# Optimization experiments

Hardware: AMD Instinct MI355X
Metric: run time of the kernel (lower is better)

## Reference

```python
import jax, jax.numpy as jnp
import numpy as np
import math

B, S, H, NH, NB = 2, 512, 128, 4, 2
D = H // NH
V_ITEMS, NCAT, NMETA, BAG, TSPAN = 50000, 1000, 16, 5, 256
EPS_EMB, EPS = 1e-5, 1e-8
NEG = -(2.0 ** 32) + 1.0


def _ln(x, g, b, eps):
    m = x.mean(-1, keepdims=True)
    v = ((x - m) ** 2).mean(-1, keepdims=True)
    return (x - m) / jnp.sqrt(v + eps) * g + b


def setup_inputs() -> dict:
    key = jax.random.key(0)
    ks = jax.random.split(key, 24)
    sc = 0.02
    inp = {}
    inp['input_ids'] = jax.random.randint(ks[0], (B, S), 0, V_ITEMS + 1)
    inp['metadata_seq'] = jax.random.normal(ks[1], (B, S, NMETA), jnp.float32)
    inp['category_seq'] = jax.random.randint(ks[2], (B, S, BAG), 0, NCAT + 1)
    inp['time_matrix'] = jax.random.randint(ks[3], (B, S, S), 0, TSPAN + 1)
    item = jax.random.normal(ks[4], (V_ITEMS + 1, H), jnp.float32) * sc
    inp['item_emb_w'] = item.at[0].set(0.0)  # padding_idx=0 cleared
    cat = jax.random.normal(ks[5], (NCAT + 1, H // 2), jnp.float32) * sc
    inp['cat_emb_w'] = cat.at[0].set(0.0)
    inp['num_W'] = jax.random.normal(ks[6], (H // 2, NMETA), jnp.float32) * sc
    inp['num_b'] = jnp.zeros((H // 2,), jnp.float32)
    inp['fusion_W'] = jax.random.normal(ks[7], (H, 2 * H), jnp.float32) * sc
    inp['fusion_b'] = jnp.zeros((H,), jnp.float32)
    inp['emb_ln_g'] = jnp.ones((H,), jnp.float32)
    inp['emb_ln_b'] = jnp.zeros((H,), jnp.float32)
    inp['pos_K_w'] = jax.random.normal(ks[8], (S, H), jnp.float32) * sc
    inp['pos_V_w'] = jax.random.normal(ks[9], (S, H), jnp.float32) * sc
    inp['time_K_w'] = jax.random.normal(ks[10], (TSPAN + 1, H), jnp.float32) * sc
    inp['time_V_w'] = jax.random.normal(ks[11], (TSPAN + 1, H), jnp.float32) * sc
    inp['attn_ln_g'] = jnp.ones((NB, H), jnp.float32)
    inp['attn_ln_b'] = jnp.zeros((NB, H), jnp.float32)
    inp['Q_W'] = jax.random.normal(ks[12], (NB, H, H), jnp.float32) * sc
    inp['Q_b'] = jnp.zeros((NB, H), jnp.float32)
    inp['K_W'] = jax.random.normal(ks[13], (NB, H, H), jnp.float32) * sc
    inp['K_b'] = jnp.zeros((NB, H), jnp.float32)
    inp['V_W'] = jax.random.normal(ks[14], (NB, H, H), jnp.float32) * sc
    inp['V_b'] = jnp.zeros((NB, H), jnp.float32)
    inp['fwd_ln_g'] = jnp.ones((NB, H), jnp.float32)
    inp['fwd_ln_b'] = jnp.zeros((NB, H), jnp.float32)
    inp['w1_W'] = jax.random.normal(ks[15], (NB, H, H), jnp.float32) * sc
    inp['w1_b'] = jnp.zeros((NB, H), jnp.float32)
    inp['w2_W'] = jax.random.normal(ks[16], (NB, H, H), jnp.float32) * sc
    inp['w2_b'] = jnp.zeros((NB, H), jnp.float32)
    inp['last_ln_g'] = jnp.ones((H,), jnp.float32)
    inp['last_ln_b'] = jnp.zeros((H,), jnp.float32)
    return inp


def reference(input_ids, metadata_seq, category_seq, time_matrix, item_emb_w,
              cat_emb_w, num_W, num_b, fusion_W, fusion_b, emb_ln_g, emb_ln_b,
              pos_K_w, pos_V_w, time_K_w, time_V_w, attn_ln_g, attn_ln_b,
              Q_W, Q_b, K_W, K_b, V_W, V_b, fwd_ln_g, fwd_ln_b,
              w1_W, w1_b, w2_W, w2_b, last_ln_g, last_ln_b):
    # ---- seq2vec ----
    item_v = item_emb_w[input_ids] * math.sqrt(H)            # [B,S,H]
    bag_mask = (category_seq != 0)                           # EmbeddingBag mean, padding_idx=0
    cat_e = cat_emb_w[category_seq] * bag_mask[..., None]    # [B,S,BAG,H/2]
    cat_v = cat_e.sum(-2) / jnp.maximum(bag_mask.sum(-1, keepdims=True), 1)
    num_v = metadata_seq @ num_W.T + num_b                   # [B,S,H/2]
    comb = jnp.concatenate([item_v, num_v, cat_v], axis=-1)  # [B,S,2H]
    vecs = _ln(comb @ fusion_W.T + fusion_b, emb_ln_g, emb_ln_b, EPS_EMB)

    # ---- vec2feats ----
    posK = pos_K_w.reshape(S, NH, D)
    posV = pos_V_w.reshape(S, NH, D)
    tK = time_K_w[time_matrix].reshape(B, S, S, NH, D)       # [B,S,S,h,d]
    tV = time_V_w[time_matrix].reshape(B, S, S, NH, D)
    timeline = (input_ids == 0)                              # [B,S]
    keep = (~timeline)[..., None].astype(vecs.dtype)
    vecs = vecs * keep
    causal = ~jnp.tril(jnp.ones((S, S), bool))               # mask where j > i
    inv_sqrt_d = 1.0 / math.sqrt(D)

    for i in range(NB):
        Qn = _ln(vecs, attn_ln_g[i], attn_ln_b[i], EPS)
        Q = (Qn @ Q_W[i].T + Q_b[i]).reshape(B, S, NH, D)
        K = (vecs @ K_W[i].T + K_b[i]).reshape(B, S, NH, D)
        V = (vecs @ V_W[i].T + V_b[i]).reshape(B, S, NH, D)
        aw = jnp.einsum('bihd,bjhd->bhij', Q, K)
        aw = aw + jnp.einsum('bihd,jhd->bhij', Q, posK)
        aw = aw + jnp.einsum('bijhd,bihd->bhij', tK, Q)
        aw = aw * inv_sqrt_d
        aw = jnp.where(timeline[:, None, :, None], NEG, aw)  # masks query rows (as in torch)
        aw = jnp.where(causal[None, None], NEG, aw)
        aw = jax.nn.softmax(aw, axis=-1)
        out = jnp.einsum('bhij,bjhd->bihd', aw, V)
        out = out + jnp.einsum('bhij,jhd->bihd', aw, posV)
        out = out + jnp.einsum('bhij,bijhd->bihd', aw, tV)
        out = out.reshape(B, S, H)
        vecs = Qn + out
        vecs = _ln(vecs, fwd_ln_g[i], fwd_ln_b[i], EPS)
        h1 = jax.nn.gelu(vecs @ w1_W[i].T + w1_b[i], approximate=False)
        vecs = vecs + (h1 @ w2_W[i].T + w2_b[i])
        vecs = vecs * keep

    return _ln(vecs, last_ln_g, last_ln_b, EPS)
```

## Files before the change

### kernel.cpp

```cpp
#include <hip/hip_runtime.h>
#include <hip/hip_cooperative_groups.h>
#include <math.h>

namespace cg = cooperative_groups;

#define Bn 2
#define Sn 512
#define Hn 128
#define NHn 4
#define Dn 32
#define BAGn 5
#define NMETAn 16
#define ROWS 1024
#define NBn 2
#define Tt 257

#define NEGF (-4294967295.0f)
#define INV_SQRT_D 0.17677669529663687f
#define SQRT_H 11.313708498984761f
#define EPS_EMB 1e-5f
#define EPSF 1e-8f

#define OFF_QN    0
#define OFF_Q     131072
#define OFF_K     262144
#define OFF_V     393216
#define OFF_O     524288

static __device__ __forceinline__ float red64(float v) {
#pragma unroll
    for (int m = 1; m < 64; m <<= 1) v += __shfl_xor(v, m, 64);
    return v;
}
static __device__ __forceinline__ float red64max(float v) {
#pragma unroll
    for (int m = 1; m < 64; m <<= 1) v = fmaxf(v, __shfl_xor(v, m, 64));
    return v;
}

static __device__ __forceinline__ void embed2(
    int r0, int t, float* sm,
    const int* __restrict__ ids, const float* __restrict__ meta,
    const int* __restrict__ cats,
    const float* __restrict__ item_w, const float* __restrict__ cat_w,
    const float* __restrict__ numW, const float* __restrict__ numb,
    const float* __restrict__ fusW, const float* __restrict__ fusb,
    const float* __restrict__ elng, const float* __restrict__ elnb,
    const float* __restrict__ alng, const float* __restrict__ alnb,
    const float* __restrict__ QW, const float* __restrict__ Qb,
    const float* __restrict__ KW, const float* __restrict__ Kb,
    const float* __restrict__ VW, const float* __restrict__ Vb,
    const float* __restrict__ posK, const float* __restrict__ posV,
    float* __restrict__ Qn, float* __restrict__ Q,
    float* __restrict__ K, float* __restrict__ V)
{
    float* combs = sm;
    float* xs    = sm + 512;
    float* qs    = sm + 768;
    float* parts = sm + 1024;
    float* pk    = sm + 1280;
    float* pv    = sm + 1536;
    float* wsum  = sm + 1792;
    int*   idl   = (int*)(sm + 1800);

    if (t < 2) idl[t] = ids[r0 + t];
    __syncthreads();
    { int r = t >> 7, c = t & 127; combs[r * 256 + c] = item_w[idl[r] * Hn + c] * SQRT_H; }
    if (t < 128) {
        int r = t >> 6, c = t & 63;
        float acc = numb[c];
#pragma unroll
        for (int m2 = 0; m2 < NMETAn; ++m2)
            acc += meta[(r0 + r) * NMETAn + m2] * numW[c * NMETAn + m2];
        combs[r * 256 + 128 + c] = acc;
    } else {
        int u = t - 128, r = u >> 6, c = u & 63;
        float ca = 0.f; int cnt = 0;
#pragma unroll
        for (int k2 = 0; k2 < BAGn; ++k2) {
            int cc2 = cats[(r0 + r) * BAGn + k2];
            if (cc2 != 0) { ca += cat_w[cc2 * 64 + c]; cnt++; }
        }
        combs[r * 256 + 192 + c] = ca / (float)(cnt > 0 ? cnt : 1);
    }
    __syncthreads();
    int h = t & 127, kh = t >> 7;
    {
        const float4* w4p = (const float4*)(fusW + h * 256 + kh * 128);
        const float* c0 = combs + kh * 128;
        const float* c1 = combs + 256 + kh * 128;
        float a0 = 0.f, a1 = 0.f, b0 = 0.f, b1 = 0.f;
#pragma unroll 16
        for (int k4 = 0; k4 < 32; ++k4) {
            float4 w4 = w4p[k4];
            int k = k4 * 4;
            a0 += c0[k] * w4.x + c0[k + 1] * w4.y;
            a1 += c0[k + 2] * w4.z + c0[k + 3] * w4.w;
            b0 += c1[k] * w4.x + c1[k + 1] * w4.y;
            b1 += c1[k + 2] * w4.z + c1[k + 3] * w4.w;
        }
        float A0 = a0 + a1, A1 = b0 + b1;
        if (kh) { parts[h] = A0; parts[128 + h] = A1; }
        __syncthreads();
        if (!kh) {
            xs[h] = A0 + parts[h] + fusb[h];
            xs[128 + h] = A1 + parts[128 + h] + fusb[h];
        }
    }
    __syncthreads();
    int w_ = t >> 6, row = w_ >> 1, l = t & 63, ch = ((w_ & 1) << 6) + l;
    float x = xs[row * 128 + ch];
    float s1 = red64(x);
    if (l == 0) wsum[w_] = s1;
    __syncthreads();
    float mean = (wsum[row * 2] + wsum[row * 2 + 1]) * (1.f / 128.f);
    float dlt = x - mean;
    float s2 = red64(dlt * dlt);
    if (l == 0) wsum[4 + w_] = s2;
    __syncthreads();
    float rstd = rsqrtf((wsum[4 + row * 2] + wsum[4 + row * 2 + 1]) * (1.f / 128.f) + EPS_EMB);
    float xv = dlt * rstd * elng[ch] + elnb[ch];
    xv = (idl[row] == 0) ? 0.f : xv;
    __syncthreads();
    xs[row * 128 + ch] = xv;
    __syncthreads();
    s1 = red64(xv);
    if (l == 0) wsum[w_] = s1;
    __syncthreads();
    mean = (wsum[row * 2] + wsum[row * 2 + 1]) * (1.f / 128.f);
    dlt = xv - mean;
    s2 = red64(dlt * dlt);
    if (l == 0) wsum[4 + w_] = s2;
    __syncthreads();
    rstd = rsqrtf((wsum[4 + row * 2] + wsum[4 + row * 2 + 1]) * (1.f / 128.f) + EPSF);
    float qn = dlt * rstd * alng[ch] + alnb[ch];
    qs[row * 128 + ch] = qn;
    Qn[(r0 + row) * 128 + ch] = qn;
    __syncthreads();
    {
        const float4* qw4 = (const float4*)(QW + h * 128 + kh * 64);
        const float4* kw4 = (const float4*)(KW + h * 128 + kh * 64);
        const float4* vw4 = (const float4*)(VW + h * 128 + kh * 64);
        const float* q0p = qs + kh * 64;
        const float* q1p = qs + 128 + kh * 64;
        const float* x0p = xs + kh * 64;
        const float* x1p = xs + 128 + kh * 64;
        float aq0 = 0, aq1 = 0, ak0 = 0, ak1 = 0, av0 = 0, av1 = 0;
#pragma unroll 8
        for (int k4 = 0; k4 < 16; ++k4) {
            float4 wq = qw4[k4], wk = kw4[k4], wv = vw4[k4];
            int k = k4 * 4;
            aq0 += q0p[k] * wq.x + q0p[k + 1] * wq.y + q0p[k + 2] * wq.z + q0p[k + 3] * wq.w;
            aq1 += q1p[k] * wq.x + q1p[k + 1] * wq.y + q1p[k + 2] * wq.z + q1p[k + 3] * wq.w;
            ak0 += x0p[k] * wk.x + x0p[k + 1] * wk.y + x0p[k + 2] * wk.z + x0p[k + 3] * wk.w;
            ak1 += x1p[k] * wk.x + x1p[k + 1] * wk.y + x1p[k + 2] * wk.z + x1p[k + 3] * wk.w;
            av0 += x0p[k] * wv.x + x0p[k + 1] * wv.y + x0p[k + 2] * wv.z + x0p[k + 3] * wv.w;
            av1 += x1p[k] * wv.x + x1p[k + 1] * wv.y + x1p[k + 2] * wv.z + x1p[k + 3] * wv.w;
        }
        if (kh) {
            parts[h] = aq0; parts[128 + h] = aq1;
            pk[h] = ak0; pk[128 + h] = ak1;
            pv[h] = av0; pv[128 + h] = av1;
        }
        __syncthreads();
        if (!kh) {
            int s0 = r0 & (Sn - 1), s1_ = (r0 + 1) & (Sn - 1);
            Q[r0 * 128 + h]       = aq0 + parts[h]       + Qb[h];
            Q[(r0 + 1) * 128 + h] = aq1 + parts[128 + h] + Qb[h];
            K[r0 * 128 + h]       = ak0 + pk[h]          + Kb[h] + posK[s0 * 128 + h];
            K[(r0 + 1) * 128 + h] = ak1 + pk[128 + h]    + Kb[h] + posK[s1_ * 128 + h];
            V[r0 * 128 + h]       = av0 + pv[h]          + Vb[h] + posV[s0 * 128 + h];
            V[(r0 + 1) * 128 + h] = av1 + pv[128 + h]    + Vb[h] + posV[s1_ * 128 + h];
        }
    }
}

static __device__ __forceinline__ void attn_phase(
    int b, int h, int i0, int t,
    const int* __restrict__ ids, const int* __restrict__ tmat,
    const float* __restrict__ Q, const float* __restrict__ K,
    const float* __restrict__ V,
    const float* __restrict__ tKw, const float* __restrict__ tVw,
    float* __restrict__ O,
    float* Kt, float* Vt, float* Stile, int* trowT,
    float* QTl, float* ql, int* tlf)
{
    __syncthreads();
    if (t < 4) tlf[t] = (ids[b * Sn + i0 + t] == 0) ? 1 : 0;
    if (t < 128) {
        int q_ = t >> 5, d = t & 31;
        ql[q_ * 33 + d] = Q[(b * Sn + i0 + q_) * Hn + h * 32 + d];
    }
    __syncthreads();

    for (int tt = t; tt < Tt; tt += 256) {
        const float4* tk4 = (const float4*)(tKw + tt * Hn + h * 32);
        float a0 = 0.f, a1 = 0.f, a2 = 0.f, a3 = 0.f;
#pragma unroll
        for (int dv = 0; dv < 8; ++dv) {
            float4 w4 = tk4[dv];
            int d = dv * 4;
            a0 += ql[d] * w4.x + ql[d + 1] * w4.y + ql[d + 2] * w4.z + ql[d + 3] * w4.w;
            a1 += ql[33 + d] * w4.x + ql[34 + d] * w4.y + ql[35 + d] * w4.z + ql[36 + d] * w4.w;
            a2 += ql[66 + d] * w4.x + ql[67 + d] * w4.y + ql[68 + d] * w4.z + ql[69 + d] * w4.w;
            a3 += ql[99 + d] * w4.x + ql[100 + d] * w4.y + ql[101 + d] * w4.z + ql[102 + d] * w4.w;
        }
        QTl[tt] = a0; QTl[260 + tt] = a1; QTl[520 + tt] = a2; QTl[780 + tt] = a3;
    }

    int tl_any = tlf[0] | tlf[1] | tlf[2] | tlf[3];
    int ntiles = tl_any ? 8 : ((i0 + 3) >> 6) + 1;

    int iq = t >> 6, jj = t & 63;
    int i_g = i0 + iq;
    int my_tl = tlf[iq];
    const int* trow = tmat + (b * Sn + i_g) * Sn;

    float qreg[32];
#pragma unroll
    for (int d = 0; d < 32; ++d) qreg[d] = ql[iq * 33 + d];

    int jq = jj >> 5, d = jj & 31;
    float m = -INFINITY, lsum = 0.f, acc = 0.f;

    for (int jt = 0; jt < ntiles; ++jt) {
        int j0 = jt * 64;
        __syncthreads();
        for (int f = t; f < 64 * 8; f += 256) {
            int jl = f >> 3, dv = f & 7;
            const float* src = K + (b * Sn + j0 + jl) * Hn + h * 32 + dv * 4;
            float4 w4 = *(const float4*)src;
            float* kd = &Kt[jl * 33 + dv * 4];
            kd[0] = w4.x; kd[1] = w4.y; kd[2] = w4.z; kd[3] = w4.w;
            float4 v4 = *(const float4*)(V + (b * Sn + j0 + jl) * Hn + h * 32 + dv * 4);
            float* vd = &Vt[jl * 33 + dv * 4];
            vd[0] = v4.x; vd[1] = v4.y; vd[2] = v4.z; vd[3] = v4.w;
        }
        __syncthreads();

        int active = my_tl || (j0 <= i_g);
        if (active) {
            int j = j0 + jj;
            float sv = NEGF;
            int tv = trow[j];
            if (!my_tl && j <= i_g) {
                float a = 0.f;
#pragma unroll
                for (int dd = 0; dd < 32; ++dd)
                    a += qreg[dd] * Kt[jj * 33 + dd];
                sv = (a + QTl[iq * 260 + tv]) * INV_SQRT_D;
            }
            float mt = red64max(sv);
            float mnew = fmaxf(m, mt);
            float alpha = expf(m - mnew);
            float p = expf(sv - mnew);
            lsum = lsum * alpha + red64(p);
            m = mnew;
            acc *= alpha;
            Stile[iq * 64 + jj] = p;
            trowT[iq * 64 + jj] = tv;
        }
        __syncthreads();
        if (active) {
            int base = jq * 32;
#pragma unroll 8
            for (int jl = base; jl < base + 32; ++jl) {
                float pp = Stile[iq * 64 + jl];
                int tv2 = trowT[iq * 64 + jl];
                acc += pp * (Vt[jl * 33 + d] + tVw[tv2 * Hn + h * 32 + d]);
            }
        }
    }

    float a2 = acc + __shfl_xor(acc, 32, 64);
    if (jj < 32)
        O[(b * Sn + i_g) * Hn + h * 32 + d] = a2 / lsum;
}

static __device__ __forceinline__ void ffn2(
    int r0, int t, float* sm,
    const int* __restrict__ ids, float* __restrict__ Qn,
    const float* __restrict__ O,
    const float* __restrict__ flng, const float* __restrict__ flnb,
    const float* __restrict__ w1W, const float* __restrict__ w1b,
    const float* __restrict__ w2W, const float* __restrict__ w2b,
    const float* __restrict__ alng, const float* __restrict__ alnb,
    const float* __restrict__ QW, const float* __restrict__ Qb,
    const float* __restrict__ KW, const float* __restrict__ Kb,
    const float* __restrict__ VW, const float* __restrict__ Vb,
    const float* __restrict__ posK, const float* __restrict__ posV,
    float* __restrict__ Q, float* __restrict__ K, float* __restrict__ V,
    const float* __restrict__ llng, const float* __restrict__ llnb,
    float* __restrict__ out, int nb, int last)
{
    float* ys    = sm;
    float* h1s   = sm + 256;
    float* parts = sm + 512;
    float* pk    = sm + 768;
    float* pv    = sm + 1024;
    float* wsum  = sm + 1280;

    ys[t] = Qn[r0 * 128 + t] + O[r0 * 128 + t];
    __syncthreads();
    int w_ = t >> 6, row = w_ >> 1, l = t & 63, ch = ((w_ & 1) << 6) + l;
    float x = ys[row * 128 + ch];
    float s1 = red64(x);
    if (l == 0) wsum[w_] = s1;
    __syncthreads();
    float mean = (wsum[row * 2] + wsum[row * 2 + 1]) * (1.f / 128.f);
    float dlt = x - mean;
    float s2 = red64(dlt * dlt);
    if (l == 0) wsum[4 + w_] = s2;
    __syncthreads();
    float rstd = rsqrtf((wsum[4 + row * 2] + wsum[4 + row * 2 + 1]) * (1.f / 128.f) + EPSF);
    float yv = dlt * rstd * flng[nb * 128 + ch] + flnb[nb * 128 + ch];
    __syncthreads();
    ys[row * 128 + ch] = yv;
    __syncthreads();

    int h = t & 127, kh = t >> 7;
    {
        const float4* w4p = (const float4*)(w1W + nb * 16384 + h * 128 + kh * 64);
        const float* y0 = ys + kh * 64;
        const float* y1 = ys + 128 + kh * 64;
        float a0 = 0.f, a1 = 0.f, b0 = 0.f, b1 = 0.f;
#pragma unroll 16
        for (int k4 = 0; k4 < 16; ++k4) {
            float4 w4 = w4p[k4];
            int k = k4 * 4;
            a0 += y0[k] * w4.x + y0[k + 1] * w4.y;
            a1 += y0[k + 2] * w4.z + y0[k + 3] * w4.w;
            b0 += y1[k] * w4.x + y1[k + 1] * w4.y;
            b1 += y1[k + 2] * w4.z + y1[k + 3] * w4.w;
        }
        float A0 = a0 + a1, A1 = b0 + b1;
        if (kh) { parts[h] = A0; parts[128 + h] = A1; }
        __syncthreads();
        if (!kh) {
            float v0 = A0 + parts[h] + w1b[nb * 128 + h];
            float v1 = A1 + parts[128 + h] + w1b[nb * 128 + h];
            h1s[h] = 0.5f * v0 * (1.f + erff(v0 * 0.70710678118654752f));
            h1s[128 + h] = 0.5f * v1 * (1.f + erff(v1 * 0.70710678118654752f));
        }
    }
    __syncthreads();
    {
        const float4* w4p = (const float4*)(w2W + nb * 16384 + h * 128 + kh * 64);
        const float* y0 = h1s + kh * 64;
        const float* y1 = h1s + 128 + kh * 64;
        float a0 = 0.f, a1 = 0.f, b0 = 0.f, b1 = 0.f;
#pragma unroll 16
        for (int k4 = 0; k4 < 16; ++k4) {
            float4 w4 = w4p[k4];
            int k = k4 * 4;
            a0 += y0[k] * w4.x + y0[k + 1] * w4.y;
            a1 += y0[k + 2] * w4.z + y0[k + 3] * w4.w;
            b0 += y1[k] * w4.x + y1[k + 1] * w4.y;
            b1 += y1[k + 2] * w4.z + y1[k + 3] * w4.w;
        }
        float A0 = a0 + a1, A1 = b0 + b1;
        __syncthreads();
        if (kh) { parts[h] = A0; parts[128 + h] = A1; }
        __syncthreads();
        if (!kh) {
            float z0 = A0 + parts[h] + w2b[nb * 128 + h] + ys[h];
            float z1 = A1 + parts[128 + h] + w2b[nb * 128 + h] + ys[128 + h];
            z0 = (ids[r0] == 0) ? 0.f : z0;
            z1 = (ids[r0 + 1] == 0) ? 0.f : z1;
            h1s[h] = z0; h1s[128 + h] = z1;
        }
    }
    __syncthreads();

    if (last) {
        x = h1s[row * 128 + ch];
        s1 = red64(x);
        if (l == 0) wsum[w_] = s1;
        __syncthreads();
        mean = (wsum[row * 2] + wsum[row * 2 + 1]) * (1.f / 128.f);
        dlt = x - mean;
        s2 = red64(dlt * dlt);
        if (l == 0) wsum[4 + w_] = s2;
        __syncthreads();
        rstd = rsqrtf((wsum[4 + row * 2] + wsum[4 + row * 2 + 1]) * (1.f / 128.f) + EPSF);
        out[(r0 + row) * 128 + ch] = dlt * rstd * llng[ch] + llnb[ch];
        return;
    }

    int nq = nb + 1;
    x = h1s[row * 128 + ch];
    s1 = red64(x);
    if (l == 0) wsum[w_] = s1;
    __syncthreads();
    mean = (wsum[row * 2] + wsum[row * 2 + 1]) * (1.f / 128.f);
    dlt = x - mean;
    s2 = red64(dlt * dlt);
    if (l == 0) wsum[4 + w_] = s2;
    __syncthreads();
    rstd = rsqrtf((wsum[4 + row * 2] + wsum[4 + row * 2 + 1]) * (1.f / 128.f) + EPSF);
    float qn = dlt * rstd * alng[nq * 128 + ch] + alnb[nq * 128 + ch];
    __syncthreads();
    ys[row * 128 + ch] = qn;
    Qn[(r0 + row) * 128 + ch] = qn;
    __syncthreads();

    {
        const float4* qw4 = (const float4*)(QW + nq * 16384 + h * 128 + kh * 64);
        const float4* kw4 = (const float4*)(KW + nq * 16384 + h * 128 + kh * 64);
        const float4* vw4 = (const float4*)(VW + nq * 16384 + h * 128 + kh * 64);
        const float* q0p = ys + kh * 64;
        const float* q1p = ys + 128 + kh * 64;
        const float* x0p = h1s + kh * 64;
        const float* x1p = h1s + 128 + kh * 64;
        float aq0 = 0, aq1 = 0, ak0 = 0, ak1 = 0, av0 = 0, av1 = 0;
#pragma unroll 8
        for (int k4 = 0; k4 < 16; ++k4) {
            float4 wq = qw4[k4], wk = kw4[k4], wv = vw4[k4];
            int k = k4 * 4;
            aq0 += q0p[k] * wq.x + q0p[k + 1] * wq.y + q0p[k + 2] * wq.z + q0p[k + 3] * wq.w;
            aq1 += q1p[k] * wq.x + q1p[k + 1] * wq.y + q1p[k + 2] * wq.z + q1p[k + 3] * wq.w;
            ak0 += x0p[k] * wk.x + x0p[k + 1] * wk.y + x0p[k + 2] * wk.z + x0p[k + 3] * wk.w;
            ak1 += x1p[k] * wk.x + x1p[k + 1] * wk.y + x1p[k + 2] * wk.z + x1p[k + 3] * wk.w;
            av0 += x0p[k] * wv.x + x0p[k + 1] * wv.y + x0p[k + 2] * wv.z + x0p[k + 3] * wv.w;
            av1 += x1p[k] * wv.x + x1p[k + 1] * wv.y + x1p[k + 2] * wv.z + x1p[k + 3] * wv.w;
        }
        if (kh) {
            parts[h] = aq0; parts[128 + h] = aq1;
            pk[h] = ak0; pk[128 + h] = ak1;
            pv[h] = av0; pv[128 + h] = av1;
        }
        __syncthreads();
        if (!kh) {
            int s0 = r0 & (Sn - 1), s1_ = (r0 + 1) & (Sn - 1);
            Q[r0 * 128 + h]       = aq0 + parts[h]       + Qb[nq * 128 + h];
            Q[(r0 + 1) * 128 + h] = aq1 + parts[128 + h] + Qb[nq * 128 + h];
            K[r0 * 128 + h]       = ak0 + pk[h]          + Kb[nq * 128 + h] + posK[s0 * 128 + h];
            K[(r0 + 1) * 128 + h] = ak1 + pk[128 + h]    + Kb[nq * 128 + h] + posK[s1_ * 128 + h];
            V[r0 * 128 + h]       = av0 + pv[h]          + Vb[nq * 128 + h] + posV[s0 * 128 + h];
            V[(r0 + 1) * 128 + h] = av1 + pv[128 + h]    + Vb[nq * 128 + h] + posV[s1_ * 128 + h];
        }
    }
}

__global__ __launch_bounds__(256, 2) void fused_kernel(
    const int* __restrict__ ids, const float* __restrict__ meta,
    const int* __restrict__ cats, const int* __restrict__ tmat,
    const float* __restrict__ item_w, const float* __restrict__ cat_w,
    const float* __restrict__ numW, const float* __restrict__ numb,
    const float* __restrict__ fusW, const float* __restrict__ fusb,
    const float* __restrict__ elng, const float* __restrict__ elnb,
    const float* __restrict__ posK, const float* __restrict__ posV,
    const float* __restrict__ tKw, const float* __restrict__ tVw,
    const float* __restrict__ alng, const float* __restrict__ alnb,
    const float* __restrict__ QW, const float* __restrict__ Qb,
    const float* __restrict__ KW, const float* __restrict__ Kb,
    const float* __restrict__ VW, const float* __restrict__ Vb,
    const float* __restrict__ flng, const float* __restrict__ flnb,
    const float* __restrict__ w1W, const float* __restrict__ w1b,
    const float* __restrict__ w2W, const float* __restrict__ w2b,
    const float* __restrict__ llng, const float* __restrict__ llnb,
    float* __restrict__ Qn, float* __restrict__ Q, float* __restrict__ K,
    float* __restrict__ V, float* __restrict__ O, float* __restrict__ out)
{
    cg::grid_group grid = cg::this_grid();
    __shared__ __align__(16) float sm[5912];
    int blk = blockIdx.x, t = threadIdx.x;
    int b8 = blk >> 6, j = blk & 63;
    int ab = b8 >> 2, ah = b8 & 3;

    embed2(blk * 2, t, sm, ids, meta, cats, item_w, cat_w, numW, numb,
           fusW, fusb, elng, elnb, alng, alnb, QW, Qb, KW, Kb, VW, Vb,
           posK, posV, Qn, Q, K, V);
    grid.sync();

    for (int nb = 0; nb < NBn; ++nb) {
        attn_phase(ab, ah, j * 4, t, ids, tmat, Q, K, V, tKw, tVw, O,
                   sm, sm + 2112, sm + 4224, (int*)(sm + 4480),
                   sm + 4736, sm + 5776, (int*)(sm + 5908));
        attn_phase(ab, ah, (127 - j) * 4, t, ids, tmat, Q, K, V, tKw, tVw, O,
                   sm, sm + 2112, sm + 4224, (int*)(sm + 4480),
                   sm + 4736, sm + 5776, (int*)(sm + 5908));
        grid.sync();
        ffn2(blk * 2, t, sm, ids, Qn, O, flng, flnb, w1W, w1b, w2W, w2b,
             alng, alnb, QW, Qb, KW, Kb, VW, Vb, posK, posV,
             Q, K, V, llng, llnb, out, nb, (nb == NBn - 1) ? 1 : 0);
        if (nb == 0) grid.sync();
    }
}

__global__ __launch_bounds__(256) void embed_qkv_kernel(
    const int* ids, const float* meta, const int* cats,
    const float* item_w, const float* cat_w, const float* numW, const float* numb,
    const float* fusW, const float* fusb, const float* elng, const float* elnb,
    const float* alng, const float* alnb,
    const float* QW, const float* Qb, const float* KW, const float* Kb,
    const float* VW, const float* Vb, const float* posK, const float* posV,
    float* Qn, float* Q, float* K, float* V)
{
    __shared__ __align__(16) float sm[1802];
    embed2(blockIdx.x * 2, threadIdx.x, sm, ids, meta, cats, item_w, cat_w,
           numW, numb, fusW, fusb, elng, elnb, alng, alnb, QW, Qb, KW, Kb,
           VW, Vb, posK, posV, Qn, Q, K, V);
}

__global__ __launch_bounds__(256) void attn_kernel(
    const int* ids, const int* tmat,
    const float* Q, const float* K, const float* V,
    const float* tKw, const float* tVw, float* O)
{
    __shared__ __align__(16) float sm[5912];
    int blk = blockIdx.x, t = threadIdx.x;
    int bh = blk & 7;
    int s  = blk >> 3;
    int g = s >> 5, r = s & 31;
    int mm;
    if      (g == 0) mm = r;
    else if (g == 1) mm = 127 - r;
    else if (g == 2) mm = 32 + r;
    else             mm = 95 - r;
    int b = bh >> 2, h = bh & 3;
    attn_phase(b, h, mm * 4, t, ids, tmat, Q, K, V, tKw, tVw, O,
               sm, sm + 2112, sm + 4224, (int*)(sm + 4480),
               sm + 4736, sm + 5776, (int*)(sm + 5908));
}

__global__ __launch_bounds__(256) void ffn_qkv_kernel(
    const int* ids, float* Qn, const float* O,
    const float* flng, const float* flnb,
    const float* w1W, const float* w1b, const float* w2W, const float* w2b,
    const float* alng, const float* alnb,
    const float* QW, const float* Qb, const float* KW, const float* Kb,
    const float* VW, const float* Vb, const float* posK, const float* posV,
    float* Q, float* K, float* V,
    const float* llng, const float* llnb, float* out, int nb, int last)
{
    __shared__ __align__(16) float sm[1288];
    ffn2(blockIdx.x * 2, threadIdx.x, sm, ids, Qn, O, flng, flnb, w1W, w1b,
         w2W, w2b, alng, alnb, QW, Qb, KW, Kb, VW, Vb, posK, posV,
         Q, K, V, llng, llnb, out, nb, last);
}

static int g_mode = -1;

extern "C" void kernel_launch(void* const* d_in, const int* in_sizes, int n_in,
                              void* d_out, int out_size, void* d_ws, size_t ws_size,
                              hipStream_t stream) {
    const int*   ids   = (const int*)  d_in[0];
    const float* meta  = (const float*)d_in[1];
    const int*   cats  = (const int*)  d_in[2];
    const int*   tmat  = (const int*)  d_in[3];
    const float* itemw = (const float*)d_in[4];
    const float* catw  = (const float*)d_in[5];
    const float* numW  = (const float*)d_in[6];
    const float* numb  = (const float*)d_in[7];
    const float* fusW  = (const float*)d_in[8];
    const float* fusb  = (const float*)d_in[9];
    const float* elng  = (const float*)d_in[10];
    const float* elnb  = (const float*)d_in[11];
    const float* posK  = (const float*)d_in[12];
    const float* posV  = (const float*)d_in[13];
    const float* tKw   = (const float*)d_in[14];
    const float* tVw   = (const float*)d_in[15];
    const float* alng  = (const float*)d_in[16];
    const float* alnb  = (const float*)d_in[17];
    const float* QW    = (const float*)d_in[18];
    const float* Qb    = (const float*)d_in[19];
    const float* KW    = (const float*)d_in[20];
    const float* Kb    = (const float*)d_in[21];
    const float* VW    = (const float*)d_in[22];
    const float* Vb    = (const float*)d_in[23];
    const float* flng  = (const float*)d_in[24];
    const float* flnb  = (const float*)d_in[25];
    const float* w1W   = (const float*)d_in[26];
    const float* w1b   = (const float*)d_in[27];
    const float* w2W   = (const float*)d_in[28];
    const float* w2b   = (const float*)d_in[29];
    const float* llng  = (const float*)d_in[30];
    const float* llnb  = (const float*)d_in[31];
    (void)in_sizes; (void)n_in; (void)out_size; (void)ws_size;

    float* ws = (float*)d_ws;
    float* Qnp = ws + OFF_QN;
    float* Qp  = ws + OFF_Q;
    float* Kp  = ws + OFF_K;
    float* Vp  = ws + OFF_V;
    float* Op  = ws + OFF_O;
    float* outp = (float*)d_out;

    if (g_mode < 0) {
        int dev = 0;
        (void)hipGetDevice(&dev);
        int coop = 0;
        (void)hipDeviceGetAttribute(&coop, hipDeviceAttributeCooperativeLaunch, dev);
        int ncu = 0;
        (void)hipDeviceGetAttribute(&ncu, hipDeviceAttributeMultiprocessorCount, dev);
        int maxb = 0;
        hipError_t oe = hipOccupancyMaxActiveBlocksPerMultiprocessor(
            &maxb, fused_kernel, 256, 0);
        g_mode = (coop && oe == hipSuccess && (long)maxb * (long)ncu >= 512) ? 1 : 0;
    }

    if (g_mode == 1) {
        void* args[] = {
            (void*)&ids, (void*)&meta, (void*)&cats, (void*)&tmat,
            (void*)&itemw, (void*)&catw, (void*)&numW, (void*)&numb,
            (void*)&fusW, (void*)&fusb, (void*)&elng, (void*)&elnb,
            (void*)&posK, (void*)&posV, (void*)&tKw, (void*)&tVw,
            (void*)&alng, (void*)&alnb, (void*)&QW, (void*)&Qb,
            (void*)&KW, (void*)&Kb, (void*)&VW, (void*)&Vb,
            (void*)&flng, (void*)&flnb, (void*)&w1W, (void*)&w1b,
            (void*)&w2W, (void*)&w2b, (void*)&llng, (void*)&llnb,
            (void*)&Qnp, (void*)&Qp, (void*)&Kp, (void*)&Vp, (void*)&Op,
            (void*)&outp
        };
        hipError_t e = hipLaunchCooperativeKernel((void*)fused_kernel,
                                                  dim3(512), dim3(256),
                                                  args, 0, stream);
        if (e == hipSuccess) return;
        g_mode = 0;
    }

    embed_qkv_kernel<<<ROWS / 2, 256, 0, stream>>>(
        ids, meta, cats, itemw, catw, numW, numb, fusW, fusb, elng, elnb,
        alng, alnb, QW, Qb, KW, Kb, VW, Vb, posK, posV, Qnp, Qp, Kp, Vp);
    for (int nb = 0; nb < NBn; ++nb) {
        attn_kernel<<<1024, 256, 0, stream>>>(ids, tmat, Qp, Kp, Vp, tKw, tVw, Op);
        ffn_qkv_kernel<<<ROWS / 2, 256, 0, stream>>>(
            ids, Qnp, Op, flng, flnb, w1W, w1b, w2W, w2b,
            alng, alnb, QW, Qb, KW, Kb, VW, Vb, posK, posV,
            Qp, Kp, Vp, llng, llnb, outp, nb, (nb == NBn - 1) ? 1 : 0);
    }
}
```

Baseline: 258.5 us.

## Use one row per block and 1024-block cooperative grid with shuffle-based attention

```diff
diff --git a/kernel.cpp b/kernel.cpp
--- a/kernel.cpp
+++ b/kernel.cpp
@@ -38,8 +38,71 @@
     return v;
 }
 
-static __device__ __forceinline__ void embed2(
-    int r0, int t, float* sm,
+static __device__ __forceinline__ float ln128(float x, int t, float* wsum, float eps) {
+    int w_ = t >> 6;
+    float s1 = red64(x);
+    if ((t & 63) == 0) wsum[w_] = s1;
+    __syncthreads();
+    float mean = (wsum[0] + wsum[1]) * (1.f / 128.f);
+    float dlt = x - mean;
+    float s2 = red64(dlt * dlt);
+    if ((t & 63) == 0) wsum[4 + w_] = s2;
+    __syncthreads();
+    float rstd = rsqrtf((wsum[4] + wsum[5]) * (1.f / 128.f) + eps);
+    return dlt * rstd;
+}
+
+static __device__ __forceinline__ float gemv_half(const float* __restrict__ W,
+                                                  const float* src, int h, int kh) {
+    const float4* w4p = (const float4*)(W + h * 128 + kh * 64);
+    const float* y0 = src + kh * 64;
+    float a0 = 0.f, a1 = 0.f;
+#pragma unroll 16
+    for (int k4 = 0; k4 < 16; ++k4) {
+        float4 w4 = w4p[k4];
+        int k = k4 * 4;
+        a0 += y0[k] * w4.x + y0[k + 1] * w4.y;
+        a1 += y0[k + 2] * w4.z + y0[k + 3] * w4.w;
+    }
+    return a0 + a1;
+}
+
+static __device__ __forceinline__ void qkv_row(
+    int row, int t, const float* qs, const float* xsrc,
+    float* parts, float* pk, float* pv,
+    const float* __restrict__ QW, const float* __restrict__ Qb,
+    const float* __restrict__ KW, const float* __restrict__ Kb,
+    const float* __restrict__ VW, const float* __restrict__ Vb,
+    const float* __restrict__ posK, const float* __restrict__ posV,
+    float* __restrict__ Q, float* __restrict__ K, float* __restrict__ V, int nq)
+{
+    int h = t & 127, kh = t >> 7;
+    const float4* qw4 = (const float4*)(QW + nq * 16384 + h * 128 + kh * 64);
+    const float4* kw4 = (const float4*)(KW + nq * 16384 + h * 128 + kh * 64);
+    const float4* vw4 = (const float4*)(VW + nq * 16384 + h * 128 + kh * 64);
+    const float* q0p = qs + kh * 64;
+    const float* x0p = xsrc + kh * 64;
+    float aq0 = 0.f, ak0 = 0.f, av0 = 0.f;
+#pragma unroll 8
+    for (int k4 = 0; k4 < 16; ++k4) {
+        float4 wq = qw4[k4], wk = kw4[k4], wv = vw4[k4];
+        int k = k4 * 4;
+        aq0 += q0p[k] * wq.x + q0p[k + 1] * wq.y + q0p[k + 2] * wq.z + q0p[k + 3] * wq.w;
+        ak0 += x0p[k] * wk.x + x0p[k + 1] * wk.y + x0p[k + 2] * wk.z + x0p[k + 3] * wk.w;
+        av0 += x0p[k] * wv.x + x0p[k + 1] * wv.y + x0p[k + 2] * wv.z + x0p[k + 3] * wv.w;
+    }
+    if (kh) { parts[h] = aq0; pk[h] = ak0; pv[h] = av0; }
+    __syncthreads();
+    if (!kh) {
+        int s0 = row & (Sn - 1);
+        Q[row * Hn + h] = aq0 + parts[h] + Qb[nq * Hn + h];
+        K[row * Hn + h] = ak0 + pk[h] + Kb[nq * Hn + h] + posK[s0 * Hn + h];
+        V[row * Hn + h] = av0 + pv[h] + Vb[nq * Hn + h] + posV[s0 * Hn + h];
+    }
+}
+
+static __device__ __forceinline__ void embed_row(
+    int row, int t, float* sm,
     const int* __restrict__ ids, const float* __restrict__ meta,
     const int* __restrict__ cats,
     const float* __restrict__ item_w, const float* __restrict__ cat_w,
@@ -55,230 +118,72 @@
     float* __restrict__ K, float* __restrict__ V)
 {
     float* combs = sm;
-    float* xs    = sm + 512;
-    float* qs    = sm + 768;
-    float* parts = sm + 1024;
-    float* pk    = sm + 1280;
-    float* pv    = sm + 1536;
-    float* wsum  = sm + 1792;
-    int*   idl   = (int*)(sm + 1800);
-
-    if (t < 2) idl[t] = ids[r0 + t];
-    __syncthreads();
-    { int r = t >> 7, c = t & 127; combs[r * 256 + c] = item_w[idl[r] * Hn + c] * SQRT_H; }
+    float* xs    = sm + 256;
+    float* qs    = sm + 384;
+    float* parts = sm + 512;
+    float* pk    = sm + 640;
+    float* pv    = sm + 768;
+    float* wsum  = sm + 896;
+
+    int id = ids[row];
+    int ch = t & 127, kh = t >> 7, h = ch;
+
     if (t < 128) {
-        int r = t >> 6, c = t & 63;
+        combs[t] = item_w[id * Hn + t] * SQRT_H;
+    } else if (t < 192) {
+        int c = t - 128;
         float acc = numb[c];
 #pragma unroll
         for (int m2 = 0; m2 < NMETAn; ++m2)
-            acc += meta[(r0 + r) * NMETAn + m2] * numW[c * NMETAn + m2];
-        combs[r * 256 + 128 + c] = acc;
+            acc += meta[row * NMETAn + m2] * numW[c * NMETAn + m2];
+        combs[128 + c] = acc;
     } else {
-        int u = t - 128, r = u >> 6, c = u & 63;
+        int c = t - 192;
         float ca = 0.f; int cnt = 0;
 #pragma unroll
         for (int k2 = 0; k2 < BAGn; ++k2) {
-            int cc2 = cats[(r0 + r) * BAGn + k2];
+            int cc2 = cats[row * BAGn + k2];
             if (cc2 != 0) { ca += cat_w[cc2 * 64 + c]; cnt++; }
         }
-        combs[r * 256 + 192 + c] = ca / (float)(cnt > 0 ? cnt : 1);
-    }
-    __syncthreads();
-    int h = t & 127, kh = t >> 7;
+        combs[192 + c] = ca / (float)(cnt > 0 ? cnt : 1);
+    }
+    __syncthreads();
+
+    float A0;
     {
         const float4* w4p = (const float4*)(fusW + h * 256 + kh * 128);
         const float* c0 = combs + kh * 128;
-        const float* c1 = combs + 256 + kh * 128;
-        float a0 = 0.f, a1 = 0.f, b0 = 0.f, b1 = 0.f;
+        float a0 = 0.f, a1 = 0.f;
 #pragma unroll 16
         for (int k4 = 0; k4 < 32; ++k4) {
             float4 w4 = w4p[k4];
             int k = k4 * 4;
             a0 += c0[k] * w4.x + c0[k + 1] * w4.y;
             a1 += c0[k + 2] * w4.z + c0[k + 3] * w4.w;
-            b0 += c1[k] * w4.x + c1[k + 1] * w4.y;
-            b1 += c1[k + 2] * w4.z + c1[k + 3] * w4.w;
         }
-        float A0 = a0 + a1, A1 = b0 + b1;
-        if (kh) { parts[h] = A0; parts[128 + h] = A1; }
-        __syncthreads();
-        if (!kh) {
-            xs[h] = A0 + parts[h] + fusb[h];
-            xs[128 + h] = A1 + parts[128 + h] + fusb[h];
-        }
-    }
-    __syncthreads();
-    int w_ = t >> 6, row = w_ >> 1, l = t & 63, ch = ((w_ & 1) << 6) + l;
-    float x = xs[row * 128 + ch];
-    float s1 = red64(x);
-    if (l == 0) wsum[w_] = s1;
-    __syncthreads();
-    float mean = (wsum[row * 2] + wsum[row * 2 + 1]) * (1.f / 128.f);
-    float dlt = x - mean;
-    float s2 = red64(dlt * dlt);
-    if (l == 0) wsum[4 + w_] = s2;
-    __syncthreads();
-    float rstd = rsqrtf((wsum[4 + row * 2] + wsum[4 + row * 2 + 1]) * (1.f / 128.f) + EPS_EMB);
-    float xv = dlt * rstd * elng[ch] + elnb[ch];
-    xv = (idl[row] == 0) ? 0.f : xv;
-    __syncthreads();
-    xs[row * 128 + ch] = xv;
-    __syncthreads();
-    s1 = red64(xv);
-    if (l == 0) wsum[w_] = s1;
-    __syncthreads();
-    mean = (wsum[row * 2] + wsum[row * 2 + 1]) * (1.f / 128.f);
-    dlt = xv - mean;
-    s2 = red64(dlt * dlt);
-    if (l == 0) wsum[4 + w_] = s2;
-    __syncthreads();
-    rstd = rsqrtf((wsum[4 + row * 2] + wsum[4 + row * 2 + 1]) * (1.f / 128.f) + EPSF);
-    float qn = dlt * rstd * alng[ch] + alnb[ch];
-    qs[row * 128 + ch] = qn;
-    Qn[(r0 + row) * 128 + ch] = qn;
-    __syncthreads();
-    {
-        const float4* qw4 = (const float4*)(QW + h * 128 + kh * 64);
-        const float4* kw4 = (const float4*)(KW + h * 128 + kh * 64);
-        const float4* vw4 = (const float4*)(VW + h * 128 + kh * 64);
-        const float* q0p = qs + kh * 64;
-        const float* q1p = qs + 128 + kh * 64;
-        const float* x0p = xs + kh * 64;
-        const float* x1p = xs + 128 + kh * 64;
-        float aq0 = 0, aq1 = 0, ak0 = 0, ak1 = 0, av0 = 0, av1 = 0;
-#pragma unroll 8
-        for (int k4 = 0; k4 < 16; ++k4) {
-            float4 wq = qw4[k4], wk = kw4[k4], wv = vw4[k4];
-            int k = k4 * 4;
-            aq0 += q0p[k] * wq.x + q0p[k + 1] * wq.y + q0p[k + 2] * wq.z + q0p[k + 3] * wq.w;
-            aq1 += q1p[k] * wq.x + q1p[k + 1] * wq.y + q1p[k + 2] * wq.z + q1p[k + 3] * wq.w;
-            ak0 += x0p[k] * wk.x + x0p[k + 1] * wk.y + x0p[k + 2] * wk.z + x0p[k + 3] * wk.w;
-            ak1 += x1p[k] * wk.x + x1p[k + 1] * wk.y + x1p[k + 2] * wk.z + x1p[k + 3] * wk.w;
-            av0 += x0p[k] * wv.x + x0p[k + 1] * wv.y + x0p[k + 2] * wv.z + x0p[k + 3] * wv.w;
-            av1 += x1p[k] * wv.x + x1p[k + 1] * wv.y + x1p[k + 2] * wv.z + x1p[k + 3] * wv.w;
-        }
-        if (kh) {
-            parts[h] = aq0; parts[128 + h] = aq1;
-            pk[h] = ak0; pk[128 + h] = ak1;
-            pv[h] = av0; pv[128 + h] = av1;
-        }
-        __syncthreads();
-        if (!kh) {
-            int s0 = r0 & (Sn - 1), s1_ = (r0 + 1) & (Sn - 1);
-            Q[r0 * 128 + h]       = aq0 + parts[h]       + Qb[h];
-            Q[(r0 + 1) * 128 + h] = aq1 + parts[128 + h] + Qb[h];
-            K[r0 * 128 + h]       = ak0 + pk[h]          + Kb[h] + posK[s0 * 128 + h];
-            K[(r0 + 1) * 128 + h] = ak1 + pk[128 + h]    + Kb[h] + posK[s1_ * 128 + h];
-            V[r0 * 128 + h]       = av0 + pv[h]          + Vb[h] + posV[s0 * 128 + h];
-            V[(r0 + 1) * 128 + h] = av1 + pv[128 + h]    + Vb[h] + posV[s1_ * 128 + h];
-        }
-    }
-}
-
-static __device__ __forceinline__ void attn_phase(
-    int b, int h, int i0, int t,
-    const int* __restrict__ ids, const int* __restrict__ tmat,
-    const float* __restrict__ Q, const float* __restrict__ K,
-    const float* __restrict__ V,
-    const float* __restrict__ tKw, const float* __restrict__ tVw,
-    float* __restrict__ O,
-    float* Kt, float* Vt, float* Stile, int* trowT,
-    float* QTl, float* ql, int* tlf)
-{
-    __syncthreads();
-    if (t < 4) tlf[t] = (ids[b * Sn + i0 + t] == 0) ? 1 : 0;
-    if (t < 128) {
-        int q_ = t >> 5, d = t & 31;
-        ql[q_ * 33 + d] = Q[(b * Sn + i0 + q_) * Hn + h * 32 + d];
-    }
-    __syncthreads();
-
-    for (int tt = t; tt < Tt; tt += 256) {
-        const float4* tk4 = (const float4*)(tKw + tt * Hn + h * 32);
-        float a0 = 0.f, a1 = 0.f, a2 = 0.f, a3 = 0.f;
-#pragma unroll
-        for (int dv = 0; dv < 8; ++dv) {
-            float4 w4 = tk4[dv];
-            int d = dv * 4;
-            a0 += ql[d] * w4.x + ql[d + 1] * w4.y + ql[d + 2] * w4.z + ql[d + 3] * w4.w;
-            a1 += ql[33 + d] * w4.x + ql[34 + d] * w4.y + ql[35 + d] * w4.z + ql[36 + d] * w4.w;
-            a2 += ql[66 + d] * w4.x + ql[67 + d] * w4.y + ql[68 + d] * w4.z + ql[69 + d] * w4.w;
-            a3 += ql[99 + d] * w4.x + ql[100 + d] * w4.y + ql[101 + d] * w4.z + ql[102 + d] * w4.w;
-        }
-        QTl[tt] = a0; QTl[260 + tt] = a1; QTl[520 + tt] = a2; QTl[780 + tt] = a3;
-    }
-
-    int tl_any = tlf[0] | tlf[1] | tlf[2] | tlf[3];
-    int ntiles = tl_any ? 8 : ((i0 + 3) >> 6) + 1;
-
-    int iq = t >> 6, jj = t & 63;
-    int i_g = i0 + iq;
-    int my_tl = tlf[iq];
-    const int* trow = tmat + (b * Sn + i_g) * Sn;
-
-    float qreg[32];
-#pragma unroll
-    for (int d = 0; d < 32; ++d) qreg[d] = ql[iq * 33 + d];
-
-    int jq = jj >> 5, d = jj & 31;
-    float m = -INFINITY, lsum = 0.f, acc = 0.f;
-
-    for (int jt = 0; jt < ntiles; ++jt) {
-        int j0 = jt * 64;
-        __syncthreads();
-        for (int f = t; f < 64 * 8; f += 256) {
-            int jl = f >> 3, dv = f & 7;
-            const float* src = K + (b * Sn + j0 + jl) * Hn + h * 32 + dv * 4;
-            float4 w4 = *(const float4*)src;
-            float* kd = &Kt[jl * 33 + dv * 4];
-            kd[0] = w4.x; kd[1] = w4.y; kd[2] = w4.z; kd[3] = w4.w;
-            float4 v4 = *(const float4*)(V + (b * Sn + j0 + jl) * Hn + h * 32 + dv * 4);
-            float* vd = &Vt[jl * 33 + dv * 4];
-            vd[0] = v4.x; vd[1] = v4.y; vd[2] = v4.z; vd[3] = v4.w;
-        }
-        __syncthreads();
-
-        int active = my_tl || (j0 <= i_g);
-        if (active) {
-            int j = j0 + jj;
-            float sv = NEGF;
-            int tv = trow[j];
-            if (!my_tl && j <= i_g) {
-                float a = 0.f;
-#pragma unroll
-                for (int dd = 0; dd < 32; ++dd)
-                    a += qreg[dd] * Kt[jj * 33 + dd];
-                sv = (a + QTl[iq * 260 + tv]) * INV_SQRT_D;
-            }
-            float mt = red64max(sv);
-            float mnew = fmaxf(m, mt);
-            float alpha = expf(m - mnew);
-            float p = expf(sv - mnew);
-            lsum = lsum * alpha + red64(p);
-            m = mnew;
-            acc *= alpha;
-            Stile[iq * 64 + jj] = p;
-            trowT[iq * 64 + jj] = tv;
-        }
-        __syncthreads();
-        if (active) {
-            int base = jq * 32;
-#pragma unroll 8
-            for (int jl = base; jl < base + 32; ++jl) {
-                float pp = Stile[iq * 64 + jl];
-                int tv2 = trowT[iq * 64 + jl];
-                acc += pp * (Vt[jl * 33 + d] + tVw[tv2 * Hn + h * 32 + d]);
-            }
-        }
-    }
-
-    float a2 = acc + __shfl_xor(acc, 32, 64);
-    if (jj < 32)
-        O[(b * Sn + i_g) * Hn + h * 32 + d] = a2 / lsum;
-}
-
-static __device__ __forceinline__ void ffn2(
-    int r0, int t, float* sm,
+        A0 = a0 + a1;
+    }
+    if (kh) parts[h] = A0;
+    __syncthreads();
+    float x = A0 + parts[h] + fusb[h];
+    float dn = ln128(x, t, wsum, EPS_EMB);
+    float xv = dn * elng[ch] + elnb[ch];
+    xv = (id == 0) ? 0.f : xv;
+    if (!kh) xs[h] = xv;
+    __syncthreads();
+
+    float x2 = xs[ch];
+    float dn2 = ln128(x2, t, wsum, EPSF);
+    float qn = dn2 * alng[ch] + alnb[ch];
+    if (!kh) { qs[h] = qn; Qn[row * Hn + h] = qn; }
+    __syncthreads();
+
+    qkv_row(row, t, qs, xs, parts, pk, pv, QW, Qb, KW, Kb, VW, Vb,
+            posK, posV, Q, K, V, 0);
+}
+
+static __device__ __forceinline__ void ffn_row(
+    int row, int t, float* sm,
     const int* __restrict__ ids, float* __restrict__ Qn,
     const float* __restrict__ O,
     const float* __restrict__ flng, const float* __restrict__ flnb,
@@ -294,155 +199,152 @@
     float* __restrict__ out, int nb, int last)
 {
     float* ys    = sm;
-    float* h1s   = sm + 256;
-    float* parts = sm + 512;
-    float* pk    = sm + 768;
-    float* pv    = sm + 1024;
-    float* wsum  = sm + 1280;
-
-    ys[t] = Qn[r0 * 128 + t] + O[r0 * 128 + t];
-    __syncthreads();
-    int w_ = t >> 6, row = w_ >> 1, l = t & 63, ch = ((w_ & 1) << 6) + l;
-    float x = ys[row * 128 + ch];
-    float s1 = red64(x);
-    if (l == 0) wsum[w_] = s1;
-    __syncthreads();
-    float mean = (wsum[row * 2] + wsum[row * 2 + 1]) * (1.f / 128.f);
-    float dlt = x - mean;
-    float s2 = red64(dlt * dlt);
-    if (l == 0) wsum[4 + w_] = s2;
-    __syncthreads();
-    float rstd = rsqrtf((wsum[4 + row * 2] + wsum[4 + row * 2 + 1]) * (1.f / 128.f) + EPSF);
-    float yv = dlt * rstd * flng[nb * 128 + ch] + flnb[nb * 128 + ch];
-    __syncthreads();
-    ys[row * 128 + ch] = yv;
-    __syncthreads();
-
-    int h = t & 127, kh = t >> 7;
-    {
-        const float4* w4p = (const float4*)(w1W + nb * 16384 + h * 128 + kh * 64);
-        const float* y0 = ys + kh * 64;
-        const float* y1 = ys + 128 + kh * 64;
-        float a0 = 0.f, a1 = 0.f, b0 = 0.f, b1 = 0.f;
-#pragma unroll 16
-        for (int k4 = 0; k4 < 16; ++k4) {
-            float4 w4 = w4p[k4];
-            int k = k4 * 4;
-            a0 += y0[k] * w4.x + y0[k + 1] * w4.y;
-            a1 += y0[k + 2] * w4.z + y0[k + 3] * w4.w;
-            b0 += y1[k] * w4.x + y1[k + 1] * w4.y;
-            b1 += y1[k + 2] * w4.z + y1[k + 3] * w4.w;
+    float* h1s   = sm + 128;
+    float* parts = sm + 256;
+    float* pk    = sm + 384;
+    float* pv    = sm + 512;
+    float* wsum  = sm + 640;
+
+    int ch = t & 127, kh = t >> 7, h = ch;
+
+    float xin = Qn[row * Hn + ch] + O[row * Hn + ch];
+    float dn = ln128(xin, t, wsum, EPSF);
+    float yv = dn * flng[nb * Hn + ch] + flnb[nb * Hn + ch];
+    if (!kh) ys[h] = yv;
+    __syncthreads();
+
+    float A0 = gemv_half(w1W + nb * 16384, ys, h, kh);
+    if (kh) parts[h] = A0;
+    __syncthreads();
+    if (!kh) {
+        float v0 = A0 + parts[h] + w1b[nb * Hn + h];
+        h1s[h] = 0.5f * v0 * (1.f + erff(v0 * 0.70710678118654752f));
+    }
+    __syncthreads();
+
+    float A1 = gemv_half(w2W + nb * 16384, h1s, h, kh);
+    if (kh) parts[h] = A1;
+    __syncthreads();
+    if (!kh) {
+        float z = A1 + parts[h] + w2b[nb * Hn + h] + ys[h];
+        z = (ids[row] == 0) ? 0.f : z;
+        h1s[h] = z;
+    }
+    __syncthreads();
+
+    float zz = h1s[ch];
+    float dn2 = ln128(zz, t, wsum, EPSF);
+
+    if (last) {
+        if (!kh) out[row * Hn + h] = dn2 * llng[h] + llnb[h];
+        return;
+    }
+
+    int nq = nb + 1;
+    float qn = dn2 * alng[nq * Hn + ch] + alnb[nq * Hn + ch];
+    if (!kh) { ys[h] = qn; Qn[row * Hn + h] = qn; }
+    __syncthreads();
+
+    qkv_row(row, t, ys, h1s, parts, pk, pv, QW, Qb, KW, Kb, VW, Vb,
+            posK, posV, Q, K, V, nq);
+}
+
+static __device__ __forceinline__ void attn_phase(
+    int b, int h, int i0, int t,
+    const int* __restrict__ ids, const int* __restrict__ tmat,
+    const float* __restrict__ Q, const float* __restrict__ K,
+    const float* __restrict__ V,
+    const float* __restrict__ tKw, const float* __restrict__ tVw,
+    float* __restrict__ O,
+    float* Kt, float* QTl, float* ql, int* tlf)
+{
+    __syncthreads();
+    if (t < 4) tlf[t] = (ids[b * Sn + i0 + t] == 0) ? 1 : 0;
+    if (t < 128) {
+        int q_ = t >> 5, d = t & 31;
+        ql[q_ * 33 + d] = Q[(b * Sn + i0 + q_) * Hn + h * 32 + d];
+    }
+    __syncthreads();
+
+    for (int tt = t; tt < Tt; tt += 256) {
+        const float4* tk4 = (const float4*)(tKw + tt * Hn + h * 32);
+        float a0 = 0.f, a1 = 0.f, a2 = 0.f, a3 = 0.f;
+#pragma unroll
+        for (int dv = 0; dv < 8; ++dv) {
+            float4 w4 = tk4[dv];
+            int d = dv * 4;
+            a0 += ql[d] * w4.x + ql[d + 1] * w4.y + ql[d + 2] * w4.z + ql[d + 3] * w4.w;
+            a1 += ql[33 + d] * w4.x + ql[34 + d] * w4.y + ql[35 + d] * w4.z + ql[36 + d] * w4.w;
+            a2 += ql[66 + d] * w4.x + ql[67 + d] * w4.y + ql[68 + d] * w4.z + ql[69 + d] * w4.w;
+            a3 += ql[99 + d] * w4.x + ql[100 + d] * w4.y + ql[101 + d] * w4.z + ql[102 + d] * w4.w;
         }
-        float A0 = a0 + a1, A1 = b0 + b1;
-        if (kh) { parts[h] = A0; parts[128 + h] = A1; }
+        QTl[tt] = a0; QTl[260 + tt] = a1; QTl[520 + tt] = a2; QTl[780 + tt] = a3;
+    }
+
+    int tl_any = tlf[0] | tlf[1] | tlf[2] | tlf[3];
+    int ntiles = tl_any ? 8 : ((i0 + 3) >> 6) + 1;
+
+    int iq = t >> 6, jj = t & 63;
+    int i_g = i0 + iq;
+    int my_tl = tlf[iq];
+    const int* trow = tmat + (b * Sn + i_g) * Sn;
+
+    float qreg[32];
+#pragma unroll
+    for (int d = 0; d < 32; ++d) qreg[d] = ql[iq * 33 + d];
+
+    int jq = jj >> 5, d = jj & 31;
+    float m = -INFINITY, lsum = 0.f, acc = 0.f;
+
+    for (int jt = 0; jt < ntiles; ++jt) {
+        int j0 = jt * 64;
         __syncthreads();
-        if (!kh) {
-            float v0 = A0 + parts[h] + w1b[nb * 128 + h];
-            float v1 = A1 + parts[128 + h] + w1b[nb * 128 + h];
-            h1s[h] = 0.5f * v0 * (1.f + erff(v0 * 0.70710678118654752f));
-            h1s[128 + h] = 0.5f * v1 * (1.f + erff(v1 * 0.70710678118654752f));
-        }
-    }
-    __syncthreads();
-    {
-        const float4* w4p = (const float4*)(w2W + nb * 16384 + h * 128 + kh * 64);
-        const float* y0 = h1s + kh * 64;
-        const float* y1 = h1s + 128 + kh * 64;
-        float a0 = 0.f, a1 = 0.f, b0 = 0.f, b1 = 0.f;
-#pragma unroll 16
-        for (int k4 = 0; k4 < 16; ++k4) {
-            float4 w4 = w4p[k4];
-            int k = k4 * 4;
-            a0 += y0[k] * w4.x + y0[k + 1] * w4.y;
-            a1 += y0[k + 2] * w4.z + y0[k + 3] * w4.w;
-            b0 += y1[k] * w4.x + y1[k + 1] * w4.y;
-            b1 += y1[k + 2] * w4.z + y1[k + 3] * w4.w;
-        }
-        float A0 = a0 + a1, A1 = b0 + b1;
-        __syncthreads();
-        if (kh) { parts[h] = A0; parts[128 + h] = A1; }
-        __syncthreads();
-        if (!kh) {
-            float z0 = A0 + parts[h] + w2b[nb * 128 + h] + ys[h];
-            float z1 = A1 + parts[128 + h] + w2b[nb * 128 + h] + ys[128 + h];
-            z0 = (ids[r0] == 0) ? 0.f : z0;
-            z1 = (ids[r0 + 1] == 0) ? 0.f : z1;
-            h1s[h] = z0; h1s[128 + h] = z1;
-        }
-    }
-    __syncthreads();
-
-    if (last) {
-        x = h1s[row * 128 + ch];
-        s1 = red64(x);
-        if (l == 0) wsum[w_] = s1;
-        __syncthreads();
-        mean = (wsum[row * 2] + wsum[row * 2 + 1]) * (1.f / 128.f);
-        dlt = x - mean;
-        s2 = red64(dlt * dlt);
-        if (l == 0) wsum[4 + w_] = s2;
-        __syncthreads();
-        rstd = rsqrtf((wsum[4 + row * 2] + wsum[4 + row * 2 + 1]) * (1.f / 128.f) + EPSF);
-        out[(r0 + row) * 128 + ch] = dlt * rstd * llng[ch] + llnb[ch];
-        return;
-    }
-
-    int nq = nb + 1;
-    x = h1s[row * 128 + ch];
-    s1 = red64(x);
-    if (l == 0) wsum[w_] = s1;
-    __syncthreads();
-    mean = (wsum[row * 2] + wsum[row * 2 + 1]) * (1.f / 128.f);
-    dlt = x - mean;
-    s2 = red64(dlt * dlt);
-    if (l == 0) wsum[4 + w_] = s2;
-    __syncthreads();
-    rstd = rsqrtf((wsum[4 + row * 2] + wsum[4 + row * 2 + 1]) * (1.f / 128.f) + EPSF);
-    float qn = dlt * rstd * alng[nq * 128 + ch] + alnb[nq * 128 + ch];
-    __syncthreads();
-    ys[row * 128 + ch] = qn;
-    Qn[(r0 + row) * 128 + ch] = qn;
-    __syncthreads();
-
-    {
-        const float4* qw4 = (const float4*)(QW + nq * 16384 + h * 128 + kh * 64);
-        const float4* kw4 = (const float4*)(KW + nq * 16384 + h * 128 + kh * 64);
-        const float4* vw4 = (const float4*)(VW + nq * 16384 + h * 128 + kh * 64);
-        const float* q0p = ys + kh * 64;
-        const float* q1p = ys + 128 + kh * 64;
-        const float* x0p = h1s + kh * 64;
-        const float* x1p = h1s + 128 + kh * 64;
-        float aq0 = 0, aq1 = 0, ak0 = 0, ak1 = 0, av0 = 0, av1 = 0;
-#pragma unroll 8
-        for (int k4 = 0; k4 < 16; ++k4) {
-            float4 wq = qw4[k4], wk = kw4[k4], wv = vw4[k4];
-            int k = k4 * 4;
-            aq0 += q0p[k] * wq.x + q0p[k + 1] * wq.y + q0p[k + 2] * wq.z + q0p[k + 3] * wq.w;
-            aq1 += q1p[k] * wq.x + q1p[k + 1] * wq.y + q1p[k + 2] * wq.z + q1p[k + 3] * wq.w;
-            ak0 += x0p[k] * wk.x + x0p[k + 1] * wk.y + x0p[k + 2] * wk.z + x0p[k + 3] * wk.w;
-            ak1 += x1p[k] * wk.x + x1p[k + 1] * wk.y + x1p[k + 2] * wk.z + x1p[k + 3] * wk.w;
-            av0 += x0p[k] * wv.x + x0p[k + 1] * wv.y + x0p[k + 2] * wv.z + x0p[k + 3] * wv.w;
-            av1 += x1p[k] * wv.x + x1p[k + 1] * wv.y + x1p[k + 2] * wv.z + x1p[k + 3] * wv.w;
-        }
-        if (kh) {
-            parts[h] = aq0; parts[128 + h] = aq1;
-            pk[h] = ak0; pk[128 + h] = ak1;
-            pv[h] = av0; pv[128 + h] = av1;
+        for (int f = t; f < 64 * 8; f += 256) {
+            int jl = f >> 3, dv = f & 7;
+            float4 w4 = *(const float4*)(K + (b * Sn + j0 + jl) * Hn + h * 32 + dv * 4);
+            float* kd = &Kt[jl * 33 + dv * 4];
+            kd[0] = w4.x; kd[1] = w4.y; kd[2] = w4.z; kd[3] = w4.w;
         }
         __syncthreads();
-        if (!kh) {
-            int s0 = r0 & (Sn - 1), s1_ = (r0 + 1) & (Sn - 1);
-            Q[r0 * 128 + h]       = aq0 + parts[h]       + Qb[nq * 128 + h];
-            Q[(r0 + 1) * 128 + h] = aq1 + parts[128 + h] + Qb[nq * 128 + h];
-            K[r0 * 128 + h]       = ak0 + pk[h]          + Kb[nq * 128 + h] + posK[s0 * 128 + h];
-            K[(r0 + 1) * 128 + h] = ak1 + pk[128 + h]    + Kb[nq * 128 + h] + posK[s1_ * 128 + h];
-            V[r0 * 128 + h]       = av0 + pv[h]          + Vb[nq * 128 + h] + posV[s0 * 128 + h];
-            V[(r0 + 1) * 128 + h] = av1 + pv[128 + h]    + Vb[nq * 128 + h] + posV[s1_ * 128 + h];
+
+        int active = my_tl || (j0 <= i_g);
+        if (active) {
+            int j = j0 + jj;
+            float sv = NEGF;
+            int tv = trow[j];
+            if (!my_tl && j <= i_g) {
+                float a = 0.f;
+#pragma unroll
+                for (int dd = 0; dd < 32; ++dd)
+                    a += qreg[dd] * Kt[jj * 33 + dd];
+                sv = (a + QTl[iq * 260 + tv]) * INV_SQRT_D;
+            }
+            float mt = red64max(sv);
+            float mnew = fmaxf(m, mt);
+            float alpha = expf(m - mnew);
+            float p = expf(sv - mnew);
+            lsum = lsum * alpha + red64(p);
+            m = mnew;
+            acc *= alpha;
+
+            const float* Vb_ = V + (size_t)(b * Sn + j0) * Hn + h * 32 + d;
+            const float* tVb_ = tVw + h * 32 + d;
+            int base = jq * 32;
+#pragma unroll 8
+            for (int jl = base; jl < base + 32; ++jl) {
+                float pp = __shfl(p, jl, 64);
+                int tv2 = __shfl(tv, jl, 64);
+                acc += pp * (Vb_[jl * Hn] + tVb_[tv2 * Hn]);
+            }
         }
     }
-}
-
-__global__ __launch_bounds__(256, 2) void fused_kernel(
+
+    float a2 = acc + __shfl_xor(acc, 32, 64);
+    if (jj < 32)
+        O[(b * Sn + i_g) * Hn + h * 32 + d] = a2 / lsum;
+}
+
+__global__ __launch_bounds__(256, 4) void fused_kernel(
     const int* __restrict__ ids, const float* __restrict__ meta,
     const int* __restrict__ cats, const int* __restrict__ tmat,
     const float* __restrict__ item_w, const float* __restrict__ cat_w,
@@ -463,32 +365,36 @@
     float* __restrict__ V, float* __restrict__ O, float* __restrict__ out)
 {
     cg::grid_group grid = cg::this_grid();
-    __shared__ __align__(16) float sm[5912];
+    __shared__ __align__(16) float sm[3288];
     int blk = blockIdx.x, t = threadIdx.x;
-    int b8 = blk >> 6, j = blk & 63;
-    int ab = b8 >> 2, ah = b8 & 3;
-
-    embed2(blk * 2, t, sm, ids, meta, cats, item_w, cat_w, numW, numb,
-           fusW, fusb, elng, elnb, alng, alnb, QW, Qb, KW, Kb, VW, Vb,
-           posK, posV, Qn, Q, K, V);
+
+    int bh = blk & 7;
+    int s  = blk >> 3;
+    int g = s >> 5, r = s & 31;
+    int mm;
+    if      (g == 0) mm = r;
+    else if (g == 1) mm = 127 - r;
+    else if (g == 2) mm = 32 + r;
+    else             mm = 95 - r;
+    int ab = bh >> 2, ah = bh & 3, ai0 = mm * 4;
+
+    embed_row(blk, t, sm, ids, meta, cats, item_w, cat_w, numW, numb,
+              fusW, fusb, elng, elnb, alng, alnb, QW, Qb, KW, Kb, VW, Vb,
+              posK, posV, Qn, Q, K, V);
     grid.sync();
 
     for (int nb = 0; nb < NBn; ++nb) {
-        attn_phase(ab, ah, j * 4, t, ids, tmat, Q, K, V, tKw, tVw, O,
-                   sm, sm + 2112, sm + 4224, (int*)(sm + 4480),
-                   sm + 4736, sm + 5776, (int*)(sm + 5908));
-        attn_phase(ab, ah, (127 - j) * 4, t, ids, tmat, Q, K, V, tKw, tVw, O,
-                   sm, sm + 2112, sm + 4224, (int*)(sm + 4480),
-                   sm + 4736, sm + 5776, (int*)(sm + 5908));
+        attn_phase(ab, ah, ai0, t, ids, tmat, Q, K, V, tKw, tVw, O,
+                   sm, sm + 2112, sm + 3152, (int*)(sm + 3284));
         grid.sync();
-        ffn2(blk * 2, t, sm, ids, Qn, O, flng, flnb, w1W, w1b, w2W, w2b,
-             alng, alnb, QW, Qb, KW, Kb, VW, Vb, posK, posV,
-             Q, K, V, llng, llnb, out, nb, (nb == NBn - 1) ? 1 : 0);
+        ffn_row(blk, t, sm, ids, Qn, O, flng, flnb, w1W, w1b, w2W, w2b,
+                alng, alnb, QW, Qb, KW, Kb, VW, Vb, posK, posV,
+                Q, K, V, llng, llnb, out, nb, (nb == NBn - 1) ? 1 : 0);
         if (nb == 0) grid.sync();
     }
 }
 
-__global__ __launch_bounds__(256) void embed_qkv_kernel(
+__global__ __launch_bounds__(256, 4) void embed1_kernel(
     const int* ids, const float* meta, const int* cats,
     const float* item_w, const float* cat_w, const float* numW, const float* numb,
     const float* fusW, const float* fusb, const float* elng, const float* elnb,
@@ -497,18 +403,18 @@
     const float* VW, const float* Vb, const float* posK, const float* posV,
     float* Qn, float* Q, float* K, float* V)
 {
-    __shared__ __align__(16) float sm[1802];
-    embed2(blockIdx.x * 2, threadIdx.x, sm, ids, meta, cats, item_w, cat_w,
-           numW, numb, fusW, fusb, elng, elnb, alng, alnb, QW, Qb, KW, Kb,
-           VW, Vb, posK, posV, Qn, Q, K, V);
-}
-
-__global__ __launch_bounds__(256) void attn_kernel(
+    __shared__ __align__(16) float sm[904];
+    embed_row(blockIdx.x, threadIdx.x, sm, ids, meta, cats, item_w, cat_w,
+              numW, numb, fusW, fusb, elng, elnb, alng, alnb, QW, Qb, KW, Kb,
+              VW, Vb, posK, posV, Qn, Q, K, V);
+}
+
+__global__ __launch_bounds__(256, 4) void attn_kernel(
     const int* ids, const int* tmat,
     const float* Q, const float* K, const float* V,
     const float* tKw, const float* tVw, float* O)
 {
-    __shared__ __align__(16) float sm[5912];
+    __shared__ __align__(16) float sm[3288];
     int blk = blockIdx.x, t = threadIdx.x;
     int bh = blk & 7;
     int s  = blk >> 3;
@@ -520,11 +426,10 @@
     else             mm = 95 - r;
     int b = bh >> 2, h = bh & 3;
     attn_phase(b, h, mm * 4, t, ids, tmat, Q, K, V, tKw, tVw, O,
-               sm, sm + 2112, sm + 4224, (int*)(sm + 4480),
-               sm + 4736, sm + 5776, (int*)(sm + 5908));
-}
-
-__global__ __launch_bounds__(256) void ffn_qkv_kernel(
+               sm, sm + 2112, sm + 3152, (int*)(sm + 3284));
+}
+
+__global__ __launch_bounds__(256, 4) void ffn1_kernel(
     const int* ids, float* Qn, const float* O,
     const float* flng, const float* flnb,
     const float* w1W, const float* w1b, const float* w2W, const float* w2b,
@@ -534,10 +439,10 @@
     float* Q, float* K, float* V,
     const float* llng, const float* llnb, float* out, int nb, int last)
 {
-    __shared__ __align__(16) float sm[1288];
-    ffn2(blockIdx.x * 2, threadIdx.x, sm, ids, Qn, O, flng, flnb, w1W, w1b,
-         w2W, w2b, alng, alnb, QW, Qb, KW, Kb, VW, Vb, posK, posV,
-         Q, K, V, llng, llnb, out, nb, last);
+    __shared__ __align__(16) float sm[648];
+    ffn_row(blockIdx.x, threadIdx.x, sm, ids, Qn, O, flng, flnb, w1W, w1b,
+            w2W, w2b, alng, alnb, QW, Qb, KW, Kb, VW, Vb, posK, posV,
+            Q, K, V, llng, llnb, out, nb, last);
 }
 
 static int g_mode = -1;
@@ -597,7 +502,7 @@
         int maxb = 0;
         hipError_t oe = hipOccupancyMaxActiveBlocksPerMultiprocessor(
             &maxb, fused_kernel, 256, 0);
-        g_mode = (coop && oe == hipSuccess && (long)maxb * (long)ncu >= 512) ? 1 : 0;
+        g_mode = (coop && oe == hipSuccess && (long)maxb * (long)ncu >= 1024) ? 1 : 0;
     }
 
     if (g_mode == 1) {
@@ -614,18 +519,18 @@
             (void*)&outp
         };
         hipError_t e = hipLaunchCooperativeKernel((void*)fused_kernel,
-                                                  dim3(512), dim3(256),
+                                                  dim3(1024), dim3(256),
                                                   args, 0, stream);
         if (e == hipSuccess) return;
         g_mode = 0;
     }
 
-    embed_qkv_kernel<<<ROWS / 2, 256, 0, stream>>>(
+    embed1_kernel<<<ROWS, 256, 0, stream>>>(
         ids, meta, cats, itemw, catw, numW, numb, fusW, fusb, elng, elnb,
         alng, alnb, QW, Qb, KW, Kb, VW, Vb, posK, posV, Qnp, Qp, Kp, Vp);
     for (int nb = 0; nb < NBn; ++nb) {
         attn_kernel<<<1024, 256, 0, stream>>>(ids, tmat, Qp, Kp, Vp, tKw, tVw, Op);
-        ffn_qkv_kernel<<<ROWS / 2, 256, 0, stream>>>(
+        ffn1_kernel<<<ROWS, 256, 0, stream>>>(
             ids, Qnp, Op, flng, flnb, w1W, w1b, w2W, w2b,
             alng, alnb, QW, Qb, KW, Kb, VW, Vb, posK, posV,
             Qp, Kp, Vp, llng, llnb, outp, nb, (nb == NBn - 1) ? 1 : 0);
```

New measurement: 391.0 us. +51.3%, slower.
